# Optimization experiments

Measured on AMD Instinct MI355X. Metric: run time of the kernel, lower is better.

Reference implementation:

```python
import jax, jax.numpy as jnp
import numpy as np
import math

EMBED = 256
NH = 8      # num_heads
NP = 4      # num_points
HD = EMBED // NH  # head_dim = 32
BS = 8
NQ = 8192
HH = 128
WW = 128


def setup_inputs() -> dict:
    key = jax.random.key(0)
    ks = jax.random.split(key, 12)
    query = jax.random.normal(ks[0], (BS, NQ, EMBED), jnp.float32)
    reference_points = jax.random.uniform(ks[1], (BS, NQ, 2), dtype=jnp.float32)
    value = jax.random.normal(ks[2], (BS, HH * WW, EMBED), jnp.float32)
    # sampling_offsets: torch init uses zero weight + structured bias (rose pattern);
    # use small random weight so the math path is exercised, keep the structured bias.
    w_off = 0.001 * jax.random.normal(ks[3], (EMBED, NH * NP * 2), jnp.float32)
    thetas = np.arange(NH, dtype=np.float32) * (2.0 * math.pi / NH)
    grid = np.stack([np.cos(thetas), np.sin(thetas)], -1)          # [NH, 2]
    grid = np.tile(grid[:, None, :], (1, NP, 1)) * np.arange(1, NP + 1, dtype=np.float32)[None, :, None]
    b_off = jnp.asarray(grid.reshape(-1), jnp.float32)              # [NH*NP*2]
    w_attn = 0.01 * jax.random.normal(ks[4], (EMBED, NH * NP), jnp.float32)
    b_attn = jnp.zeros((NH * NP,), jnp.float32)
    xav = 1.0 / math.sqrt(EMBED)
    w_val = xav * jax.random.normal(ks[5], (EMBED, EMBED), jnp.float32)
    b_val = jnp.zeros((EMBED,), jnp.float32)
    w_out = xav * jax.random.normal(ks[6], (EMBED, EMBED), jnp.float32)
    b_out = jnp.zeros((EMBED,), jnp.float32)
    return {"query": query, "reference_points": reference_points, "value": value,
            "w_off": w_off, "b_off": b_off, "w_attn": w_attn, "b_attn": b_attn,
            "w_val": w_val, "b_val": b_val, "w_out": w_out, "b_out": b_out,
            "H": HH, "W": WW}


def _deform_attn(query, reference_points, value, w_off, b_off, w_attn, b_attn,
                 w_val, b_val, w_out, b_out, H, W):
    bs, nq, _ = query.shape
    # value projection -> [bs, nh, H*W, hd]
    v = (value @ w_val + b_val).reshape(bs, H * W, NH, HD).transpose(0, 2, 1, 3)
    # offsets and attention weights
    off = (query @ w_off + b_off).reshape(bs, nq, NH, NP, 2)
    attn = jax.nn.softmax((query @ w_attn + b_attn).reshape(bs, nq, NH, NP), axis=-1)
    norm = jnp.array([W, H], dtype=query.dtype)
    loc = reference_points[:, :, None, None, :] + off / norm       # [bs,nq,nh,np,2] in [0,1]
    # grid_sample, align_corners=False: pixel = loc*size - 0.5  (x <-> W, y <-> H)
    px = (loc[..., 0] * W - 0.5).transpose(0, 2, 1, 3).reshape(bs, NH, nq * NP)
    py = (loc[..., 1] * H - 0.5).transpose(0, 2, 1, 3).reshape(bs, NH, nq * NP)
    x0 = jnp.floor(px); y0 = jnp.floor(py)
    wx = px - x0; wy = py - y0
    x0i = x0.astype(jnp.int32); y0i = y0.astype(jnp.int32)

    def gather(xi, yi):
        # padding_mode='zeros': out-of-range corners contribute 0
        mask = ((xi >= 0) & (xi < W) & (yi >= 0) & (yi < H)).astype(v.dtype)
        idx = jnp.clip(yi, 0, H - 1) * W + jnp.clip(xi, 0, W - 1)   # [bs,nh,K]
        g = jnp.take_along_axis(v, idx[..., None], axis=2)          # [bs,nh,K,hd]
        return g * mask[..., None]

    samp = (((1 - wx) * (1 - wy))[..., None] * gather(x0i, y0i)
            + (wx * (1 - wy))[..., None] * gather(x0i + 1, y0i)
            + ((1 - wx) * wy)[..., None] * gather(x0i, y0i + 1)
            + (wx * wy)[..., None] * gather(x0i + 1, y0i + 1))      # [bs,nh,nq*np,hd]
    samp = samp.reshape(bs, NH, nq, NP, HD)
    aw = attn.transpose(0, 2, 1, 3)                                 # [bs,nh,nq,np]
    out = jnp.einsum('bhqpd,bhqp->bqhd', samp, aw).reshape(bs, nq, EMBED)
    return out @ w_out + b_out


def reference(query, reference_points, value, w_off, b_off, w_attn, b_attn,
              w_val, b_val, w_out, b_out, H, W):
    return _deform_attn(query, reference_points, value, w_off, b_off, w_attn, b_attn,
                        w_val, b_val, w_out, b_out, H, W)
```

## Files before the change

### kernel.cpp

```cpp
#include <hip/hip_runtime.h>
#include <stdint.h>

#define NQ 8192
#define BSZ 8
#define NH 8
#define NP 4
#define HD 32
#define EMBED 256
#define IMG 128
#define NPIX (IMG*IMG)

typedef __attribute__((ext_vector_type(8))) short short8v;
typedef __attribute__((ext_vector_type(4))) float f32x4;

static __device__ __forceinline__ float bf2f(uint32_t u) {
    union { uint32_t i; float f; } x; x.i = u << 16; return x.f;
}
static __device__ __forceinline__ uint16_t f2bf(float f) {
    union { float f; uint32_t i; } x; x.f = f;
    uint32_t r = x.i + 0x7fffu + ((x.i >> 16) & 1u);
    return (uint16_t)(r >> 16);
}
static __device__ __forceinline__ uint32_t cvtpk(float lo, float hi) {
    uint32_t r;
    asm("v_cvt_pk_bf16_f32 %0, %1, %2" : "=v"(r) : "v"(lo), "v"(hi));
    return r;
}
static __device__ __forceinline__ void gload_lds16(const void* g, void* l) {
    __builtin_amdgcn_global_load_lds(
        (const __attribute__((address_space(1))) unsigned int*)g,
        (__attribute__((address_space(3))) unsigned int*)l, 16, 0, 0);
}

#define WAITV(n)   asm volatile("s_waitcnt vmcnt(" #n ")" ::: "memory")
#define WAITLGKM() asm volatile("s_waitcnt lgkmcnt(0)" ::: "memory")
#define BAR()      __builtin_amdgcn_s_barrier()
#define CLOBBER()  asm volatile("" ::: "memory")

static __device__ __forceinline__ void waitv_n(int n) {
    switch (n) {
        case 0: WAITV(0); break;  case 1: WAITV(1); break;
        case 2: WAITV(2); break;  case 3: WAITV(3); break;
        case 4: WAITV(4); break;  case 5: WAITV(5); break;
        case 6: WAITV(6); break;  case 8: WAITV(8); break;
        default: WAITV(10); break;
    }
}

__global__ void pack_w(const float* __restrict__ w_val, const float* __restrict__ w_out,
                       const float* __restrict__ w_off, const float* __restrict__ w_attn,
                       uint16_t* __restrict__ wTval, uint16_t* __restrict__ wTout,
                       uint16_t* __restrict__ wTcat) {
    int k = blockIdx.x;
    int n = threadIdx.x;
    wTval[n * 256 + k] = f2bf(w_val[k * 256 + n]);
    wTout[n * 256 + k] = f2bf(w_out[k * 256 + n]);
    if (n < 64)       wTcat[n * 256 + k]        = f2bf(w_off[k * 64 + n]);
    else if (n < 96)  wTcat[n * 256 + k]        = f2bf(w_attn[k * 32 + (n - 64)]);
}

template<bool A_F32, bool OUT_F32, bool PLANE, int STRIPES>
__global__ __launch_bounds__(512, 2)
void gemm_pk(const void* __restrict__ Ap, const uint16_t* __restrict__ BT,
             void* __restrict__ Cp, const float* __restrict__ bias) {
    constexpr int TILEB = A_F32 ? 16384 : 8192;
    constexpr int NR    = 131072 / TILEB;
    constexpr int T     = STRIPES * 4;
    constexpr int LPT   = A_F32 ? 2 : 1;
    __shared__ char SMEM[131072 + (PLANE ? 32768 : 0)];
    char* ring = SMEM;
    const int tid = threadIdx.x, w = tid >> 6, l = tid & 63;
    const int stripe0 = blockIdx.x * STRIPES;

    auto stageA = [&](int slot, int t) {
        const int gr0 = (stripe0 + (t >> 2)) * 64 + (t & 3) * 16;
        if constexpr (A_F32) {
#pragma unroll
            for (int c = 0; c < 2; ++c) {
                int loff = c * 8192 + tid * 16;
                int row = loff >> 10, x = loff & 1023;
                const char* src = (const char*)Ap + (size_t)(gr0 + row) * 1024
                                  + (x ^ ((row & 7) << 4));
                gload_lds16(src, ring + slot * 16384 + c * 8192 + w * 1024);
            }
        } else {
            int loff = tid * 16;
            int row = loff >> 9, x = loff & 511;
            const char* src = (const char*)Ap + (size_t)(gr0 + row) * 512
                              + (x ^ ((row & 7) << 4));
            gload_lds16(src, ring + slot * 8192 + w * 1024);
        }
    };

#pragma unroll
    for (int c = 0; c < 16; ++c) {
        int loff = c * 8192 + tid * 16;
        int row = loff >> 9, x = loff & 511;
        const char* src = (const char*)BT + (size_t)row * 512 + (x ^ ((row & 7) << 4));
        gload_lds16(src, SMEM + c * 8192 + w * 1024);
    }
    WAITV(0);
    BAR();
    CLOBBER();
    short8v breg[2][8];
#pragma unroll
    for (int n = 0; n < 2; ++n) {
        int col = w * 32 + n * 16 + (l & 15);
        const char* base = SMEM + col * 512;
        const int sz = (col & 7) << 4;
#pragma unroll
        for (int k = 0; k < 8; ++k)
            breg[n][k] = *(const short8v*)(base + ((k * 64 + (l >> 4) * 16) ^ sz));
    }
    WAITLGKM();
    BAR();
    CLOBBER();
#pragma unroll
    for (int t = 0; t < 6; ++t) stageA(t & (NR - 1), t);

    for (int st = 0; st < STRIPES; ++st) {
        f32x4 acc[4][2] = {};
#pragma unroll
        for (int s = 0; s < 4; ++s) {
            const int t = st * 4 + s;
            const int rem = T - 1 - t;
            waitv_n((rem < 5 ? rem : 5) * LPT);
            BAR();
            CLOBBER();
            if (t + 6 < T) stageA((t + 6) & (NR - 1), t + 6);
            const int slot = t & (NR - 1);
            short8v a[8];
            const int sz = (l & 7) << 4;
            if constexpr (A_F32) {
                const char* base = ring + slot * 16384 + (l & 15) * 1024;
#pragma unroll
                for (int k = 0; k < 8; ++k) {
                    int off = k * 128 + (l >> 4) * 32;
                    f32x4 lo = *(const f32x4*)(base + (off ^ sz));
                    f32x4 hi = *(const f32x4*)(base + ((off + 16) ^ sz));
                    union { uint32_t u[4]; short8v s8; } pk;
                    pk.u[0] = cvtpk(lo[0], lo[1]); pk.u[1] = cvtpk(lo[2], lo[3]);
                    pk.u[2] = cvtpk(hi[0], hi[1]); pk.u[3] = cvtpk(hi[2], hi[3]);
                    a[k] = pk.s8;
                }
            } else {
                const char* base = ring + slot * 8192 + (l & 15) * 512;
#pragma unroll
                for (int k = 0; k < 8; ++k)
                    a[k] = *(const short8v*)(base + ((k * 64 + (l >> 4) * 16) ^ sz));
            }
#pragma unroll
            for (int k = 0; k < 8; ++k)
#pragma unroll
                for (int n = 0; n < 2; ++n)
                    acc[s][n] = __builtin_amdgcn_mfma_f32_16x16x32_bf16(a[k], breg[n][k], acc[s][n], 0, 0, 0);
        }

        const int gr0 = (stripe0 + st) * 64;
        if constexpr (PLANE) {
            char* Cs = SMEM + 131072;
#pragma unroll
            for (int s = 0; s < 4; ++s)
#pragma unroll
                for (int n = 0; n < 2; ++n) {
                    int lcol = w * 32 + n * 16 + (l & 15);
                    float bv = bias[lcol];
#pragma unroll
                    for (int r = 0; r < 4; ++r) {
                        int lrow = s * 16 + (l >> 4) * 4 + r;
                        *(uint16_t*)(Cs + ((lrow * 512 + lcol * 2) ^ ((lrow & 7) << 4)))
                            = f2bf(acc[s][n][r] + bv);
                    }
                }
            WAITLGKM();
            BAR();
            CLOBBER();
            const int b_ = gr0 >> 14, pix0 = gr0 & 16383;
            char* pb = (char*)Cp + (((size_t)(b_ * 8 + w)) << 20) + (size_t)pix0 * 64;
#pragma unroll
            for (int i = 0; i < 4; ++i) {
                int fb = i * 1024 + l * 16;
                int lrow = fb >> 6, x = w * 64 + (fb & 63);
                uint4 d = *(const uint4*)(Cs + ((lrow * 512 + x) ^ ((lrow & 7) << 4)));
                *(uint4*)(pb + (size_t)lrow * 64 + (fb & 63)) = d;
            }
        } else {
#pragma unroll
            for (int s = 0; s < 4; ++s)
#pragma unroll
                for (int n = 0; n < 2; ++n) {
                    int col = w * 32 + n * 16 + (l & 15);
                    float bv = bias[col];
#pragma unroll
                    for (int r = 0; r < 4; ++r) {
                        int gr = gr0 + s * 16 + (l >> 4) * 4 + r;
                        float val = acc[s][n][r] + bv;
                        if constexpr (OUT_F32)
                            ((float*)Cp)[(size_t)gr * 256 + col] = val;
                        else
                            ((uint16_t*)Cp)[(size_t)gr * 256 + col] = f2bf(val);
                    }
                }
        }
    }
}

__global__ __launch_bounds__(256, 2)
void proj_kernel(const float* __restrict__ Q, const uint16_t* __restrict__ WTcat,
                 const float* __restrict__ b_off, const float* __restrict__ b_attn,
                 const float* __restrict__ refp,
                 float* __restrict__ locs, float* __restrict__ attnw) {
    __shared__ uint16_t Bs[96 * 256];
    __shared__ uint16_t As[64 * 256];
    const int tid = threadIdx.x, w = tid >> 6, l = tid & 63;
    const int blk = blockIdx.x;

#pragma unroll
    for (int c = 0; c < 12; ++c) {
        int loff = (w * 12 + c) * 1024;
        int lofl = loff + l * 16;
        int row = lofl >> 9, colb = lofl & 511;
        const char* src = (const char*)WTcat + (size_t)row * 512 + (colb ^ ((row & 7) << 4));
        gload_lds16(src, (char*)Bs + loff);
    }
#pragma unroll
    for (int c = 0; c < 8; ++c) {
        int loff = tid * 16 + c * 4096;
        int row = loff >> 9, colb = loff & 511;
        const float* src = Q + (size_t)(blk * 64 + row) * 256 + (colb >> 1);
        float4 f0 = *(const float4*)src;
        float4 f1 = *(const float4*)(src + 4);
        uint4 pk;
        pk.x = (uint32_t)f2bf(f0.x) | ((uint32_t)f2bf(f0.y) << 16);
        pk.y = (uint32_t)f2bf(f0.z) | ((uint32_t)f2bf(f0.w) << 16);
        pk.z = (uint32_t)f2bf(f1.x) | ((uint32_t)f2bf(f1.y) << 16);
        pk.w = (uint32_t)f2bf(f1.z) | ((uint32_t)f2bf(f1.w) << 16);
        *(uint4*)((char*)As + row * 512 + (colb ^ ((row & 7) << 4))) = pk;
    }
    __syncthreads();

    f32x4 acc[6] = {};
    const int arow = w * 16 + (l & 15);
#pragma unroll
    for (int ks = 0; ks < 8; ++ks) {
        const int kb = ks * 64 + (l >> 4) * 16;
        short8v a = *(const short8v*)((const char*)As + arow * 512 + (kb ^ ((arow & 7) << 4)));
#pragma unroll
        for (int n = 0; n < 6; ++n) {
            int col = n * 16 + (l & 15);
            short8v b = *(const short8v*)((const char*)Bs + col * 512 + (kb ^ ((col & 7) << 4)));
            acc[n] = __builtin_amdgcn_mfma_f32_16x16x32_bf16(a, b, acc[n], 0, 0, 0);
        }
    }
    __syncthreads();
    float* scores = (float*)As;
#pragma unroll
    for (int n = 0; n < 6; ++n)
#pragma unroll
        for (int r = 0; r < 4; ++r)
            scores[(w * 16 + (l >> 4) * 4 + r) * 96 + n * 16 + (l & 15)] = acc[n][r];
    __syncthreads();

    for (int it = tid; it < 512; it += 256) {
        int row = it >> 3, h = it & 7;
        int gq = blk * 64 + row;
        int b = gq >> 13, q = gq & 8191;
        size_t itemH = ((size_t)(b * 8 + h) << 13) | q;
        float s0 = scores[row * 96 + 64 + h * 4 + 0] + b_attn[h * 4 + 0];
        float s1 = scores[row * 96 + 64 + h * 4 + 1] + b_attn[h * 4 + 1];
        float s2 = scores[row * 96 + 64 + h * 4 + 2] + b_attn[h * 4 + 2];
        float s3 = scores[row * 96 + 64 + h * 4 + 3] + b_attn[h * 4 + 3];
        float mx = fmaxf(fmaxf(s0, s1), fmaxf(s2, s3));
        float e0 = __expf(s0 - mx), e1 = __expf(s1 - mx);
        float e2 = __expf(s2 - mx), e3 = __expf(s3 - mx);
        float inv = 1.0f / (e0 + e1 + e2 + e3);
        float rx = refp[gq * 2 + 0] * 128.0f - 0.5f;
        float ry = refp[gq * 2 + 1] * 128.0f - 0.5f;
        float ew[4] = { e0, e1, e2, e3 };
#pragma unroll
        for (int p = 0; p < 4; ++p) {
            float ox = scores[row * 96 + h * 8 + p * 2 + 0] + b_off[h * 8 + p * 2 + 0];
            float oy = scores[row * 96 + h * 8 + p * 2 + 1] + b_off[h * 8 + p * 2 + 1];
            locs[itemH * 8 + p * 2 + 0] = rx + ox;
            locs[itemH * 8 + p * 2 + 1] = ry + oy;
            attnw[itemH * 4 + p] = ew[p] * inv;
        }
    }
}

__global__ __launch_bounds__(256)
void sample_kernel(const uint16_t* __restrict__ v, const float* __restrict__ locs,
                   const float* __restrict__ attnw, uint16_t* __restrict__ oatt) {
    const int bid = blockIdx.x;
    const int h = bid & 7;
    const int rest = bid >> 3;
    const int b = rest >> 7;
    const int chunk = rest & 127;
    const int qloc = threadIdx.x >> 2;
    const int dg = threadIdx.x & 3;
    const int q = chunk * 64 + qloc;
    const size_t itemH = ((size_t)(b * 8 + h) << 13) | q;
    const char* plane = (const char*)v + ((size_t)(b * 8 + h) << 20);

    float4 l01 = ((const float4*)locs)[itemH * 2 + 0];
    float4 l23 = ((const float4*)locs)[itemH * 2 + 1];
    float4 aw4 = ((const float4*)attnw)[itemH];
    float pxs[4] = { l01.x, l01.z, l23.x, l23.z };
    float pys[4] = { l01.y, l01.w, l23.y, l23.w };
    float aws[4] = { aw4.x, aw4.y, aw4.z, aw4.w };

    float acc[8] = {};
#pragma unroll
    for (int p = 0; p < 4; ++p) {
        float px = pxs[p], py = pys[p], aw = aws[p];
        float fx = floorf(px), fy = floorf(py);
        float wx = px - fx, wy = py - fy;
        int x0 = (int)fx, y0 = (int)fy;
#pragma unroll
        for (int cy = 0; cy < 2; ++cy) {
            int yy = y0 + cy;
            float wyv = cy ? wy : 1.f - wy;
            bool yok = (unsigned)yy < (unsigned)IMG;
            int yc = min(max(yy, 0), IMG - 1);
#pragma unroll
            for (int cx = 0; cx < 2; ++cx) {
                int xx = x0 + cx;
                bool ok = yok && ((unsigned)xx < (unsigned)IMG);
                int xc = min(max(xx, 0), IMG - 1);
                float wgt = ok ? aw * (cx ? wx : 1.f - wx) * wyv : 0.f;
                const uint4 u = *(const uint4*)(plane + ((size_t)(yc * IMG + xc) << 6) + dg * 16);
                acc[0] += wgt * bf2f(u.x & 0xffffu);
                acc[1] += wgt * bf2f(u.x >> 16);
                acc[2] += wgt * bf2f(u.y & 0xffffu);
                acc[3] += wgt * bf2f(u.y >> 16);
                acc[4] += wgt * bf2f(u.z & 0xffffu);
                acc[5] += wgt * bf2f(u.z >> 16);
                acc[6] += wgt * bf2f(u.w & 0xffffu);
                acc[7] += wgt * bf2f(u.w >> 16);
            }
        }
    }
    const size_t bq = (size_t)b * NQ + q;
    uint4 out;
    out.x = (uint32_t)f2bf(acc[0]) | ((uint32_t)f2bf(acc[1]) << 16);
    out.y = (uint32_t)f2bf(acc[2]) | ((uint32_t)f2bf(acc[3]) << 16);
    out.z = (uint32_t)f2bf(acc[4]) | ((uint32_t)f2bf(acc[5]) << 16);
    out.w = (uint32_t)f2bf(acc[6]) | ((uint32_t)f2bf(acc[7]) << 16);
    *(uint4*)((char*)oatt + (bq * 256 + h * 32 + dg * 8) * 2) = out;
}

extern "C" void kernel_launch(void* const* d_in, const int* in_sizes, int n_in,
                              void* d_out, int out_size, void* d_ws, size_t ws_size,
                              hipStream_t stream) {
    const float* query  = (const float*)d_in[0];
    const float* refp   = (const float*)d_in[1];
    const float* value  = (const float*)d_in[2];
    const float* w_off  = (const float*)d_in[3];
    const float* b_off  = (const float*)d_in[4];
    const float* w_attn = (const float*)d_in[5];
    const float* b_attn = (const float*)d_in[6];
    const float* w_val  = (const float*)d_in[7];
    const float* b_val  = (const float*)d_in[8];
    const float* w_out  = (const float*)d_in[9];
    const float* b_out  = (const float*)d_in[10];

    char* ws = (char*)d_ws;
    uint16_t* v     = (uint16_t*)(ws);
    uint16_t* oatt  = (uint16_t*)(ws + (64u << 20));
    float*    locs  = (float*)(ws + (96u << 20));
    float*    attnw = (float*)(ws + (112u << 20));
    uint16_t* wTval = (uint16_t*)(ws + (120u << 20));
    uint16_t* wTout = (uint16_t*)(ws + (120u << 20) + 131072);
    uint16_t* wTcat = (uint16_t*)(ws + (120u << 20) + 262144);

    pack_w<<<256, 256, 0, stream>>>(w_val, w_out, w_off, w_attn, wTval, wTout, wTcat);
    gemm_pk<true, false, true, 8><<<256, 512, 0, stream>>>(value, wTval, v, b_val);
    proj_kernel<<<1024, 256, 0, stream>>>(query, wTcat, b_off, b_attn, refp, locs, attnw);
    sample_kernel<<<8192, 256, 0, stream>>>(v, locs, attnw, oatt);
    gemm_pk<false, true, false, 4><<<256, 512, 0, stream>>>(oatt, wTout, (float*)d_out, b_out);
}
```

Measured before the change: 138.9 us.

## Replace value-projection GEMM with dedicated kernel using direct B loads and smaller LDS

Adds a specialized value-projection kernel (vproj2) that loads the B operand straight from global memory into registers instead of staging it through LDS. Each block handles 256 rows with a 4-slot, 2-ahead prefetch ring and writes the head-planar bf16 output every 32 rows. LDS use drops to 80KB and launch bounds target more resident blocks with 512 blocks, aiming to cut the large B-staging prologue and raise occupancy. gemm_pk is reduced to the bf16-input, fp32-output variant. The shallower prefetch depth and more frequent epilogue barriers may expose more memory latency.

```diff
diff --git a/kernel.cpp b/kernel.cpp
--- a/kernel.cpp
+++ b/kernel.cpp
@@ -59,37 +59,117 @@
     else if (n < 96)  wTcat[n * 256 + k]        = f2bf(w_attn[k * 32 + (n - 64)]);
 }
 
-template<bool A_F32, bool OUT_F32, bool PLANE, int STRIPES>
+__global__ __launch_bounds__(512, 4)
+void vproj2(const float* __restrict__ Ap, const uint16_t* __restrict__ BT,
+            uint16_t* __restrict__ Vp, const float* __restrict__ bias) {
+    __shared__ char SMEM[81920];
+    char* ring = SMEM;
+    char* Cs = SMEM + 65536;
+    const int tid = threadIdx.x, w = tid >> 6, l = tid & 63;
+    const int bid = blockIdx.x;
+    const int row0 = bid * 256;
+
+    auto stageA = [&](int t) {
+        const int gr0 = row0 + t * 16;
+#pragma unroll
+        for (int c = 0; c < 2; ++c) {
+            int loff = c * 8192 + tid * 16;
+            int row = loff >> 10, x = loff & 1023;
+            const char* src = (const char*)Ap + (size_t)(gr0 + row) * 1024
+                              + (x ^ ((row & 7) << 4));
+            gload_lds16(src, ring + (t & 3) * 16384 + c * 8192 + w * 1024);
+        }
+    };
+
+    short8v breg[2][8];
+    float bv[2];
+#pragma unroll
+    for (int n = 0; n < 2; ++n) {
+        int col = w * 32 + n * 16 + (l & 15);
+        bv[n] = bias[col];
+        const char* bb = (const char*)BT + (size_t)col * 512 + (l >> 4) * 16;
+#pragma unroll
+        for (int k = 0; k < 8; ++k)
+            breg[n][k] = *(const short8v*)(bb + k * 64);
+    }
+
+    stageA(0); stageA(1);
+
+    f32x4 acc[2][2] = {};
+#pragma unroll
+    for (int t = 0; t < 16; ++t) {
+        if (t <= 1 || t == 15) { WAITV(2); } else { WAITV(4); }
+        BAR(); CLOBBER();
+        if (t + 2 < 16) stageA(t + 2);
+        const char* base = ring + (t & 3) * 16384 + (l & 15) * 1024;
+        const int sz = (l & 7) << 4;
+        short8v a[8];
+#pragma unroll
+        for (int k = 0; k < 8; ++k) {
+            int off = k * 128 + (l >> 4) * 32;
+            f32x4 lo = *(const f32x4*)(base + (off ^ sz));
+            f32x4 hi = *(const f32x4*)(base + ((off + 16) ^ sz));
+            union { uint32_t u[4]; short8v s8; } pk;
+            pk.u[0] = cvtpk(lo[0], lo[1]); pk.u[1] = cvtpk(lo[2], lo[3]);
+            pk.u[2] = cvtpk(hi[0], hi[1]); pk.u[3] = cvtpk(hi[2], hi[3]);
+            a[k] = pk.s8;
+        }
+        const int s = t & 1;
+#pragma unroll
+        for (int k = 0; k < 8; ++k)
+#pragma unroll
+            for (int n = 0; n < 2; ++n)
+                acc[s][n] = __builtin_amdgcn_mfma_f32_16x16x32_bf16(a[k], breg[n][k], acc[s][n], 0, 0, 0);
+        if (s == 1) {
+            const int gr0 = row0 + (t - 1) * 16;
+#pragma unroll
+            for (int ss = 0; ss < 2; ++ss)
+#pragma unroll
+                for (int n = 0; n < 2; ++n) {
+                    int lcol = w * 32 + n * 16 + (l & 15);
+#pragma unroll
+                    for (int r = 0; r < 4; ++r) {
+                        int lrow = ss * 16 + (l >> 4) * 4 + r;
+                        *(uint16_t*)(Cs + ((lrow * 512 + lcol * 2) ^ ((lrow & 7) << 4)))
+                            = f2bf(acc[ss][n][r] + bv[n]);
+                    }
+                }
+            WAITLGKM();
+            BAR(); CLOBBER();
+            const int b_ = gr0 >> 14, pix0 = gr0 & 16383;
+#pragma unroll
+            for (int i = 0; i < 2; ++i) {
+                int fb = i * 8192 + tid * 16;
+                int lrow = fb >> 9, x = fb & 511;
+                uint4 d = *(const uint4*)(Cs + ((lrow * 512 + x) ^ ((lrow & 7) << 4)));
+                int h_off = x >> 6, dbyte = x & 63;
+                *(uint4*)((char*)Vp + (((size_t)(b_ * 8 + h_off)) << 20)
+                          + (size_t)(pix0 + lrow) * 64 + dbyte) = d;
+            }
+            acc[0][0] = f32x4{0.f,0.f,0.f,0.f}; acc[0][1] = f32x4{0.f,0.f,0.f,0.f};
+            acc[1][0] = f32x4{0.f,0.f,0.f,0.f}; acc[1][1] = f32x4{0.f,0.f,0.f,0.f};
+        }
+    }
+}
+
+template<int STRIPES>
 __global__ __launch_bounds__(512, 2)
 void gemm_pk(const void* __restrict__ Ap, const uint16_t* __restrict__ BT,
              void* __restrict__ Cp, const float* __restrict__ bias) {
-    constexpr int TILEB = A_F32 ? 16384 : 8192;
-    constexpr int NR    = 131072 / TILEB;
-    constexpr int T     = STRIPES * 4;
-    constexpr int LPT   = A_F32 ? 2 : 1;
-    __shared__ char SMEM[131072 + (PLANE ? 32768 : 0)];
+    constexpr int NR = 16;
+    constexpr int T  = STRIPES * 4;
+    __shared__ char SMEM[131072];
     char* ring = SMEM;
     const int tid = threadIdx.x, w = tid >> 6, l = tid & 63;
     const int stripe0 = blockIdx.x * STRIPES;
 
     auto stageA = [&](int slot, int t) {
         const int gr0 = (stripe0 + (t >> 2)) * 64 + (t & 3) * 16;
-        if constexpr (A_F32) {
-#pragma unroll
-            for (int c = 0; c < 2; ++c) {
-                int loff = c * 8192 + tid * 16;
-                int row = loff >> 10, x = loff & 1023;
-                const char* src = (const char*)Ap + (size_t)(gr0 + row) * 1024
-                                  + (x ^ ((row & 7) << 4));
-                gload_lds16(src, ring + slot * 16384 + c * 8192 + w * 1024);
-            }
-        } else {
-            int loff = tid * 16;
-            int row = loff >> 9, x = loff & 511;
-            const char* src = (const char*)Ap + (size_t)(gr0 + row) * 512
-                              + (x ^ ((row & 7) << 4));
-            gload_lds16(src, ring + slot * 8192 + w * 1024);
-        }
+        int loff = tid * 16;
+        int row = loff >> 9, x = loff & 511;
+        const char* src = (const char*)Ap + (size_t)(gr0 + row) * 512
+                          + (x ^ ((row & 7) << 4));
+        gload_lds16(src, ring + slot * 8192 + w * 1024);
     };
 
 #pragma unroll
@@ -124,84 +204,36 @@
         for (int s = 0; s < 4; ++s) {
             const int t = st * 4 + s;
             const int rem = T - 1 - t;
-            waitv_n((rem < 5 ? rem : 5) * LPT);
+            waitv_n(rem < 5 ? rem : 5);
             BAR();
             CLOBBER();
             if (t + 6 < T) stageA((t + 6) & (NR - 1), t + 6);
             const int slot = t & (NR - 1);
             short8v a[8];
             const int sz = (l & 7) << 4;
-            if constexpr (A_F32) {
-                const char* base = ring + slot * 16384 + (l & 15) * 1024;
-#pragma unroll
-                for (int k = 0; k < 8; ++k) {
-                    int off = k * 128 + (l >> 4) * 32;
-                    f32x4 lo = *(const f32x4*)(base + (off ^ sz));
-                    f32x4 hi = *(const f32x4*)(base + ((off + 16) ^ sz));
-                    union { uint32_t u[4]; short8v s8; } pk;
-                    pk.u[0] = cvtpk(lo[0], lo[1]); pk.u[1] = cvtpk(lo[2], lo[3]);
-                    pk.u[2] = cvtpk(hi[0], hi[1]); pk.u[3] = cvtpk(hi[2], hi[3]);
-                    a[k] = pk.s8;
-                }
-            } else {
-                const char* base = ring + slot * 8192 + (l & 15) * 512;
-#pragma unroll
-                for (int k = 0; k < 8; ++k)
-                    a[k] = *(const short8v*)(base + ((k * 64 + (l >> 4) * 16) ^ sz));
-            }
+            const char* base = ring + slot * 8192 + (l & 15) * 512;
+#pragma unroll
+            for (int k = 0; k < 8; ++k)
+                a[k] = *(const short8v*)(base + ((k * 64 + (l >> 4) * 16) ^ sz));
 #pragma unroll
             for (int k = 0; k < 8; ++k)
 #pragma unroll
                 for (int n = 0; n < 2; ++n)
                     acc[s][n] = __builtin_amdgcn_mfma_f32_16x16x32_bf16(a[k], breg[n][k], acc[s][n], 0, 0, 0);
         }
-
         const int gr0 = (stripe0 + st) * 64;
-        if constexpr (PLANE) {
-            char* Cs = SMEM + 131072;
-#pragma unroll
-            for (int s = 0; s < 4; ++s)
-#pragma unroll
-                for (int n = 0; n < 2; ++n) {
-                    int lcol = w * 32 + n * 16 + (l & 15);
-                    float bv = bias[lcol];
-#pragma unroll
-                    for (int r = 0; r < 4; ++r) {
-                        int lrow = s * 16 + (l >> 4) * 4 + r;
-                        *(uint16_t*)(Cs + ((lrow * 512 + lcol * 2) ^ ((lrow & 7) << 4)))
-                            = f2bf(acc[s][n][r] + bv);
-                    }
+#pragma unroll
+        for (int s = 0; s < 4; ++s)
+#pragma unroll
+            for (int n = 0; n < 2; ++n) {
+                int col = w * 32 + n * 16 + (l & 15);
+                float bv = bias[col];
+#pragma unroll
+                for (int r = 0; r < 4; ++r) {
+                    int gr = gr0 + s * 16 + (l >> 4) * 4 + r;
+                    ((float*)Cp)[(size_t)gr * 256 + col] = acc[s][n][r] + bv;
                 }
-            WAITLGKM();
-            BAR();
-            CLOBBER();
-            const int b_ = gr0 >> 14, pix0 = gr0 & 16383;
-            char* pb = (char*)Cp + (((size_t)(b_ * 8 + w)) << 20) + (size_t)pix0 * 64;
-#pragma unroll
-            for (int i = 0; i < 4; ++i) {
-                int fb = i * 1024 + l * 16;
-                int lrow = fb >> 6, x = w * 64 + (fb & 63);
-                uint4 d = *(const uint4*)(Cs + ((lrow * 512 + x) ^ ((lrow & 7) << 4)));
-                *(uint4*)(pb + (size_t)lrow * 64 + (fb & 63)) = d;
             }
-        } else {
-#pragma unroll
-            for (int s = 0; s < 4; ++s)
-#pragma unroll
-                for (int n = 0; n < 2; ++n) {
-                    int col = w * 32 + n * 16 + (l & 15);
-                    float bv = bias[col];
-#pragma unroll
-                    for (int r = 0; r < 4; ++r) {
-                        int gr = gr0 + s * 16 + (l >> 4) * 4 + r;
-                        float val = acc[s][n][r] + bv;
-                        if constexpr (OUT_F32)
-                            ((float*)Cp)[(size_t)gr * 256 + col] = val;
-                        else
-                            ((uint16_t*)Cp)[(size_t)gr * 256 + col] = f2bf(val);
-                    }
-                }
-        }
     }
 }
 
@@ -374,8 +406,8 @@
     uint16_t* wTcat = (uint16_t*)(ws + (120u << 20) + 262144);
 
     pack_w<<<256, 256, 0, stream>>>(w_val, w_out, w_off, w_attn, wTval, wTout, wTcat);
-    gemm_pk<true, false, true, 8><<<256, 512, 0, stream>>>(value, wTval, v, b_val);
+    vproj2<<<512, 512, 0, stream>>>(value, wTval, v, b_val);
     proj_kernel<<<1024, 256, 0, stream>>>(query, wTcat, b_off, b_attn, refp, locs, attnw);
     sample_kernel<<<8192, 256, 0, stream>>>(v, locs, attnw, oatt);
-    gemm_pk<false, true, false, 4><<<256, 512, 0, stream>>>(oatt, wTout, (float*)d_out, b_out);
-}
+    gemm_pk<4><<<256, 512, 0, stream>>>(oatt, wTout, (float*)d_out, b_out);
+}
```

Result: slower. 223.1 us (+60.7%).
